# Kernel tuning notes

Measured on AMD Instinct MI355X. Metric: run time of the kernel, lower is better.

The kernel has to match this reference:

```python
import jax, jax.numpy as jnp
import numpy as np

EMBED = 1024
HEADS = 16
DH = EMBED // HEADS
B, S = 2, 2048


def setup_inputs() -> dict:
    key = jax.random.key(0)
    ks = jax.random.split(key, 12)
    inp = {
        "k": jax.random.normal(ks[0], (B, S, EMBED), jnp.float32),
        "q": jax.random.normal(ks[1], (B, S, EMBED), jnp.float32),
        "v": jax.random.normal(ks[2], (B, S, EMBED), jnp.float32),
        "mask": jax.random.randint(ks[3], (B, 1, S, S), 0, 2, jnp.int32),
        # per-head projections (shared across heads, as in the torch module)
        "Wk": jax.random.normal(ks[4], (DH, DH), jnp.float32) / np.sqrt(DH),
        "bk": jnp.zeros((DH,), jnp.float32),
        "Wq": jax.random.normal(ks[5], (DH, DH), jnp.float32) / np.sqrt(DH),
        "bq": jnp.zeros((DH,), jnp.float32),
        "Wv": jax.random.normal(ks[6], (DH, DH), jnp.float32) / np.sqrt(DH),
        "bv": jnp.zeros((DH,), jnp.float32),
        "Wo": jax.random.normal(ks[7], (EMBED, EMBED), jnp.float32) / np.sqrt(EMBED),
        "bo": jnp.zeros((EMBED,), jnp.float32),
    }
    return inp


def reference(k, q, v, mask, Wk, bk, Wq, bq, Wv, bv, Wo, bo):
    b, s, _ = k.shape
    sq = q.shape[1]
    # [B,S,H,dh]
    kh = k.reshape(b, s, HEADS, DH)
    qh = q.reshape(b, sq, HEADS, DH)
    vh = v.reshape(b, s, HEADS, DH)
    # per-head linear (weight shared across heads): x @ W.T + b
    kh = kh @ Wk.T + bk
    qh = qh @ Wq.T + bq
    vh = vh @ Wv.T + bv
    # scores [B,H,Sq,Sk]
    product = jnp.einsum("bqhd,bkhd->bhqk", qh, kh)
    # masked_fill BEFORE scaling, as in the original
    product = jnp.where(mask == 0, jnp.float32(-1e20), product)
    product = product / np.sqrt(DH)
    scores = jax.nn.softmax(product, axis=-1)
    ctx = jnp.einsum("bhqk,bkhd->bqhd", scores, vh).reshape(b, sq, EMBED)
    return ctx @ Wo.T + bo
```

## Files before the change

### kernel.cpp

```cpp
#include <hip/hip_runtime.h>
#include <hip/hip_bf16.h>
#include <math.h>

#define EMBED 1024
#define HEADS 16
#define DH    64
#define BATCH 2
#define SEQ   2048

typedef __attribute__((ext_vector_type(8))) short bf16x8;
typedef __attribute__((ext_vector_type(4))) short bf16x4;
typedef __attribute__((ext_vector_type(4))) float f32x4;
typedef unsigned long long u64;

#define QSCALE 0.1803368801111244f

static __device__ __forceinline__ unsigned short f2bf(float x) {
    unsigned u = __builtin_bit_cast(unsigned, x);
    return (unsigned short)((u + 0x7fffu + ((u >> 16) & 1u)) >> 16);
}
static __device__ __forceinline__ unsigned pk2bf(float a, float b) {
    union { __hip_bfloat162 h2; unsigned u; } c;
    c.h2 = __float22bfloat162_rn(make_float2(a, b));
    return c.u;
}
static __device__ __forceinline__ void gl_lds16(const void* g, void* l) {
    __builtin_amdgcn_global_load_lds(
        (const __attribute__((address_space(1))) void*)g,
        (__attribute__((address_space(3))) void*)l, 16, 0, 0);
}
static __device__ __forceinline__ bf16x8 cvt8(const float* p) {
    float4 a = ((const float4*)p)[0];
    float4 b = ((const float4*)p)[1];
    union { unsigned u[4]; bf16x8 v; } c;
    c.u[0] = pk2bf(a.x, a.y); c.u[1] = pk2bf(a.z, a.w);
    c.u[2] = pk2bf(b.x, b.y); c.u[3] = pk2bf(b.z, b.w);
    return c.v;
}

__global__ __launch_bounds__(256) void proj_mfma(
    const float* __restrict__ q, const float* __restrict__ k, const float* __restrict__ v,
    const float* __restrict__ Wq, const float* __restrict__ bq,
    const float* __restrict__ Wk, const float* __restrict__ bk,
    const float* __restrict__ Wv, const float* __restrict__ bv,
    unsigned short* __restrict__ qh, unsigned short* __restrict__ kh,
    unsigned short* __restrict__ vt,
    const int* __restrict__ mask, u64* __restrict__ bits,
    const float* __restrict__ Wo, unsigned short* __restrict__ Wob)
{
    const int blk   = blockIdx.x;
    const int which = blockIdx.y;
    const int t     = threadIdx.x;

    if (which == 3) {
        if (blk < 512) {
            const int idx = blk * 256 + t;
            const int4* src = (const int4*)(mask + (size_t)idx * 64);
            u64 wb = 0;
#pragma unroll
            for (int u = 0; u < 16; ++u) {
                int4 m = src[u];
                u64 nib = (m.x != 0 ? 1ull : 0) | (m.y != 0 ? 2ull : 0) |
                          (m.z != 0 ? 4ull : 0) | (m.w != 0 ? 8ull : 0);
                wb |= nib << (u * 4);
            }
            bits[idx] = wb;
        } else {
            const int i = ((blk - 512) * 256 + t) * 8;
            float4 a = ((const float4*)(Wo + i))[0];
            float4 b = ((const float4*)(Wo + i))[1];
            unsigned o32[4] = {pk2bf(a.x, a.y), pk2bf(a.z, a.w),
                               pk2bf(b.x, b.y), pk2bf(b.z, b.w)};
            *(uint4*)(Wob + i) = *(uint4*)o32;
        }
        return;
    }

    const float* x; const float* W; const float* bias;
    if (which == 0)      { x = q; W = Wq; bias = bq; }
    else if (which == 1) { x = k; W = Wk; bias = bk; }
    else                 { x = v; W = Wv; bias = bv; }

    __shared__ unsigned short Ws[64 * 72];

    const int w    = t >> 6;
    const int lane = t & 63;
    const int l15  = lane & 15;
    const int quad = lane >> 4;

    const int sr = t >> 2, sp = t & 3;
    {
        const float* wsrc = W + (size_t)sr * 64 + sp * 16;
        unsigned o32[8];
#pragma unroll
        for (int u4 = 0; u4 < 4; ++u4) {
            float4 a = ((const float4*)wsrc)[u4];
            o32[u4 * 2 + 0] = pk2bf(a.x, a.y);
            o32[u4 * 2 + 1] = pk2bf(a.z, a.w);
        }
        *(uint4*)&Ws[sr * 72 + sp * 16]     = *(uint4*)&o32[0];
        *(uint4*)&Ws[sr * 72 + sp * 16 + 8] = *(uint4*)&o32[4];
    }

    if (which == 2) {
        const int bh = blk >> 5;
        const int st = blk & 31;
        const int b  = bh >> 4, h = bh & 15;
        const int s  = st * 64 + w * 16 + l15;

        const float* xrow = x + ((size_t)(b * SEQ + s)) * EMBED + h * DH;
        const bf16x8 bx0 = cvt8(xrow + quad * 8);
        const bf16x8 bx1 = cvt8(xrow + 32 + quad * 8);

        __syncthreads();

#pragma unroll
        for (int nt = 0; nt < 4; ++nt) {
            bf16x8 aw0 = *(const bf16x8*)&Ws[(nt * 16 + l15) * 72 + quad * 8];
            bf16x8 aw1 = *(const bf16x8*)&Ws[(nt * 16 + l15) * 72 + 32 + quad * 8];
            f32x4 a = {0, 0, 0, 0};
            a = __builtin_amdgcn_mfma_f32_16x16x32_bf16(aw0, bx0, a, 0, 0, 0);
            a = __builtin_amdgcn_mfma_f32_16x16x32_bf16(aw1, bx1, a, 0, 0, 0);
#pragma unroll
            for (int r = 0; r < 4; ++r) {
                const int d = nt * 16 + quad * 4 + r;
                vt[((size_t)bh * DH + d) * SEQ + s] = f2bf(a[r] + bias[d]);
            }
        }
        return;
    }

    const float oscale = (which == 0) ? QSCALE : 1.0f;
    unsigned short* out = (which == 0) ? qh : kh;

    const float* xrow = x + ((size_t)blk * 64 + w * 16 + l15) * 64;
    const bf16x8 af0 = cvt8(xrow + quad * 8);
    const bf16x8 af1 = cvt8(xrow + 32 + quad * 8);

    __syncthreads();

    f32x4 acc[4];
#pragma unroll
    for (int nt = 0; nt < 4; ++nt) {
        bf16x8 bf0 = *(const bf16x8*)&Ws[(nt * 16 + l15) * 72 + quad * 8];
        bf16x8 bf1 = *(const bf16x8*)&Ws[(nt * 16 + l15) * 72 + 32 + quad * 8];
        f32x4 a = {0, 0, 0, 0};
        a = __builtin_amdgcn_mfma_f32_16x16x32_bf16(af0, bf0, a, 0, 0, 0);
        a = __builtin_amdgcn_mfma_f32_16x16x32_bf16(af1, bf1, a, 0, 0, 0);
        acc[nt] = a;
    }

    const int bsidx = blk * 4 + w;
    const int b = bsidx >> 11, s = bsidx & 2047;
#pragma unroll
    for (int nt = 0; nt < 4; ++nt) {
        const int d = nt * 16 + l15;
        const float bb = bias[d];
#pragma unroll
        for (int r = 0; r < 4; ++r) {
            const int h = quad * 4 + r;
            out[(((size_t)b * HEADS + h) * SEQ + s) * DH + d] =
                f2bf((acc[nt][r] + bb) * oscale);
        }
    }
}

__global__ __launch_bounds__(256, 4) void attn_kernel(
    const unsigned short* __restrict__ qh, const unsigned short* __restrict__ kh,
    const unsigned short* __restrict__ vt, const u64* __restrict__ mbits,
    unsigned short* __restrict__ ctx)
{
    const int bid = blockIdx.x;
    const int bh  = bid & 31;
    const int q0  = (bid >> 5) * 64;
    const int b   = bh >> 4;

    __shared__ unsigned char smem[32768];

    const int t    = threadIdx.x;
    const int w    = t >> 6;
    const int lane = t & 63;
    const int l15  = lane & 15;
    const int quad = lane >> 4;

    const int srow   = lane >> 3;
    const int schunk = (lane & 7) ^ srow;

    const unsigned short* qb = qh + ((size_t)bh * SEQ + q0 + w * 16 + l15) * DH + quad * 8;
    const bf16x8 qf0 = *(const bf16x8*)qb;
    const bf16x8 qf1 = *(const bf16x8*)(qb + 32);

    f32x4 O[4];
#pragma unroll
    for (int dt = 0; dt < 4; ++dt) O[dt] = f32x4{0, 0, 0, 0};
    f32x4 Osum = {0, 0, 0, 0};
    const bf16x4 ones = {(short)0x3F80, (short)0x3F80, (short)0x3F80, (short)0x3F80};

    const unsigned short* kbase = kh + (size_t)bh * SEQ * DH
                                  + (size_t)srow * DH + schunk * 8;
    const unsigned short* vbase = vt + (size_t)bh * DH * SEQ
                                  + (size_t)srow * SEQ + schunk * 8;
    const u64* mrow = mbits + ((size_t)b * SEQ + q0 + w * 16 + l15) * (SEQ / 64);

    if (w < 2) {
        unsigned char* Kd = smem;
#pragma unroll
        for (int j = 0; j < 4; ++j) {
            const int i = w * 4 + j;
            gl_lds16(kbase + (size_t)i * 8 * DH, Kd + i * 1024);
        }
    } else {
        unsigned char* Vd = smem + 8192;
#pragma unroll
        for (int j = 0; j < 4; ++j) {
            const int i = (w - 2) * 4 + j;
            gl_lds16(vbase + (size_t)i * 8 * SEQ, Vd + i * 1024);
        }
    }
    u64 pm = mrow[0];
    __syncthreads();

    for (int kt = 0; kt < 32; ++kt) {
        if (kt < 31) {
            const int bn = (kt + 1) & 1;
            if (w < 2) {
                unsigned char* Kd = smem + bn * 16384;
                const unsigned short* g0 = kbase + (size_t)(kt + 1) * 64 * DH;
#pragma unroll
                for (int j = 0; j < 4; ++j) {
                    const int i = w * 4 + j;
                    gl_lds16(g0 + (size_t)i * 8 * DH, Kd + i * 1024);
                }
            } else {
                unsigned char* Vd = smem + bn * 16384 + 8192;
                const unsigned short* g0 = vbase + (kt + 1) * 64;
#pragma unroll
                for (int j = 0; j < 4; ++j) {
                    const int i = (w - 2) * 4 + j;
                    gl_lds16(g0 + (size_t)i * 8 * SEQ, Vd + i * 1024);
                }
            }
        }
        const u64 mb = pm;
        if (kt < 31) pm = mrow[kt + 1];

        const unsigned short* KtH = (const unsigned short*)(smem + (kt & 1) * 16384);
        const unsigned short* VtH = KtH + 4096;

        const u64 mq = mb >> (quad * 4);
        bf16x4 p[4];
        const int rx = l15 & 7;
#pragma unroll
        for (int st = 0; st < 4; ++st) {
            const int r = st * 16 + l15;
            bf16x8 kf0 = *(const bf16x8*)&KtH[r * 64 + ((quad ^ rx)) * 8];
            bf16x8 kf1 = *(const bf16x8*)&KtH[r * 64 + ((quad ^ rx) ^ 4) * 8];
            f32x4 sa = {0, 0, 0, 0};
            sa = __builtin_amdgcn_mfma_f32_16x16x32_bf16(kf0, qf0, sa, 0, 0, 0);
            sa = __builtin_amdgcn_mfma_f32_16x16x32_bf16(kf1, qf1, sa, 0, 0, 0);
            const unsigned nib = (unsigned)(mq >> (st * 16)) & 0xFu;
            float p0 = (nib & 1u) ? exp2f(sa[0]) : 0.f;
            float p1 = (nib & 2u) ? exp2f(sa[1]) : 0.f;
            float p2 = (nib & 4u) ? exp2f(sa[2]) : 0.f;
            float p3 = (nib & 8u) ? exp2f(sa[3]) : 0.f;
            union { unsigned u2[2]; bf16x4 v; } pu;
            pu.u2[0] = pk2bf(p0, p1);
            pu.u2[1] = pk2bf(p2, p3);
            p[st] = pu.v;
            Osum = __builtin_amdgcn_mfma_f32_16x16x16bf16_1k(p[st], ones, Osum, 0, 0, 0);
        }

#pragma unroll
        for (int dt = 0; dt < 4; ++dt) {
            const int d = dt * 16 + l15;
            const int dx = l15 & 7;
#pragma unroll
            for (int st = 0; st < 4; ++st) {
                const int ch = (st * 2 + (quad >> 1)) ^ dx;
                bf16x4 vb = *(const bf16x4*)&VtH[d * 64 + ch * 8 + (quad & 1) * 4];
                O[dt] = __builtin_amdgcn_mfma_f32_16x16x16bf16_1k(p[st], vb, O[dt], 0, 0, 0);
            }
        }
        __syncthreads();
    }

    float inv[4];
#pragma unroll
    for (int r = 0; r < 4; ++r) inv[r] = 1.0f / Osum[r];
#pragma unroll
    for (int r = 0; r < 4; ++r) {
        const int row = q0 + w * 16 + quad * 4 + r;
        unsigned short* dst = ctx + ((size_t)bh * SEQ + row) * DH + l15;
#pragma unroll
        for (int dt = 0; dt < 4; ++dt)
            dst[dt * 16] = f2bf(O[dt][r] * inv[r]);
    }
}

__global__ __launch_bounds__(256, 4) void outproj_mfma(
    const unsigned short* __restrict__ ctx, const unsigned short* __restrict__ Wob,
    const float* __restrict__ bo, float* __restrict__ out)
{
    const int n0 = blockIdx.x * 64;
    const int m0 = blockIdx.y * 64;
    const int b  = m0 / SEQ;
    const int s0 = m0 % SEQ;

    __shared__ unsigned char smem[32768];

    const int t    = threadIdx.x;
    const int w    = t >> 6;
    const int lane = t & 63;
    const int l15  = lane & 15;
    const int quad = lane >> 4;
    const int srow   = lane >> 3;
    const int schunk = (lane & 7) ^ srow;

    const unsigned short* abase = ctx + ((size_t)b * HEADS * SEQ + s0 + srow) * DH + schunk * 8;
    const unsigned short* wbase = Wob + (size_t)(n0 + srow) * EMBED + schunk * 8;

    f32x4 acc[4] = {f32x4{0,0,0,0}, f32x4{0,0,0,0}, f32x4{0,0,0,0}, f32x4{0,0,0,0}};

    {
        unsigned char* Ab = smem;
        unsigned char* Wb = smem + 8192;
#pragma unroll
        for (int j = 0; j < 4; ++j) {
            const int idx = w * 4 + j;
            if (idx < 8)
                gl_lds16(abase + (size_t)idx * 8 * DH, Ab + idx * 1024);
            else
                gl_lds16(wbase + (size_t)(idx - 8) * 8 * EMBED, Wb + (idx - 8) * 1024);
        }
    }
    __syncthreads();

    for (int kt = 0; kt < 16; ++kt) {
        if (kt < 15) {
            const int ktn = kt + 1;
            unsigned char* Ab = smem + (ktn & 1) * 16384;
            unsigned char* Wb = Ab + 8192;
#pragma unroll
            for (int j = 0; j < 4; ++j) {
                const int idx = w * 4 + j;
                if (idx < 8)
                    gl_lds16(abase + (size_t)ktn * SEQ * DH + (size_t)idx * 8 * DH,
                             Ab + idx * 1024);
                else
                    gl_lds16(wbase + (size_t)(idx - 8) * 8 * EMBED + ktn * 64,
                             Wb + (idx - 8) * 1024);
            }
        }

        const unsigned short* At = (const unsigned short*)(smem + (kt & 1) * 16384);
        const unsigned short* Wt = At + 4096;
        const int rx = l15 & 7;
        const int c0 = ((quad ^ rx)) * 8;

        bf16x8 bf0 = *(const bf16x8*)&Wt[(w * 16 + l15) * 64 + c0];
        bf16x8 bf1 = *(const bf16x8*)&Wt[(w * 16 + l15) * 64 + (c0 ^ 32)];
#pragma unroll
        for (int mt = 0; mt < 4; ++mt) {
            bf16x8 af0 = *(const bf16x8*)&At[(mt * 16 + l15) * 64 + c0];
            bf16x8 af1 = *(const bf16x8*)&At[(mt * 16 + l15) * 64 + (c0 ^ 32)];
            acc[mt] = __builtin_amdgcn_mfma_f32_16x16x32_bf16(af0, bf0, acc[mt], 0, 0, 0);
            acc[mt] = __builtin_amdgcn_mfma_f32_16x16x32_bf16(af1, bf1, acc[mt], 0, 0, 0);
        }
        __syncthreads();
    }

    const float bv = bo[n0 + w * 16 + l15];
#pragma unroll
    for (int mt = 0; mt < 4; ++mt) {
#pragma unroll
        for (int r = 0; r < 4; ++r) {
            out[(size_t)(m0 + mt * 16 + quad * 4 + r) * EMBED + n0 + w * 16 + l15] =
                acc[mt][r] + bv;
        }
    }
}

extern "C" void kernel_launch(void* const* d_in, const int* in_sizes, int n_in,
                              void* d_out, int out_size, void* d_ws, size_t ws_size,
                              hipStream_t stream) {
    const float* k    = (const float*)d_in[0];
    const float* q    = (const float*)d_in[1];
    const float* v    = (const float*)d_in[2];
    const int*   mask = (const int*)  d_in[3];
    const float* Wk   = (const float*)d_in[4];
    const float* bk   = (const float*)d_in[5];
    const float* Wq   = (const float*)d_in[6];
    const float* bq   = (const float*)d_in[7];
    const float* Wv   = (const float*)d_in[8];
    const float* bv   = (const float*)d_in[9];
    const float* Wo   = (const float*)d_in[10];
    const float* bo   = (const float*)d_in[11];
    float* out = (float*)d_out;

    const size_t TEN = (size_t)BATCH * HEADS * SEQ * DH;
    unsigned short* qh_bf = (unsigned short*)d_ws;
    unsigned short* kh_bf = qh_bf + TEN;
    unsigned short* vt_bf = kh_bf + TEN;
    unsigned short* ctxb  = vt_bf + TEN;
    unsigned short* Wob   = ctxb + TEN;
    u64*            mbits = (u64*)(Wob + EMBED * EMBED);

    proj_mfma<<<dim3(1024, 4), 256, 0, stream>>>(
        q, k, v, Wq, bq, Wk, bk, Wv, bv,
        qh_bf, kh_bf, vt_bf, mask, mbits, Wo, Wob);
    attn_kernel<<<dim3((SEQ / 64) * BATCH * HEADS), 256, 0, stream>>>(
        qh_bf, kh_bf, vt_bf, mbits, ctxb);
    outproj_mfma<<<dim3(EMBED / 64, BATCH * SEQ / 64), 256, 0, stream>>>(
        ctxb, Wob, bo, out);
}
```

Measured before the change: 240.0 us.

## Pre-swizzle K into MFMA fragment layout and read it directly from global

The projection kernel now writes K in a packed layout laid out per 16-row group and 8-column chunk, so that each lane of the attention kernel can load its MFMA operand fragments straight from global memory (through L2/L1) instead of staging K tiles in LDS. Only V remains double-buffered in LDS, which halves the shared-memory footprint and the number of async copies per iteration. The compute section is also wrapped in s_setprio to raise wave priority. The cost is that K loads now come from cache with no software prefetch, so global load latency may be exposed in the QK step.

```diff
diff --git a/kernel.cpp b/kernel.cpp
--- a/kernel.cpp
+++ b/kernel.cpp
@@ -43,7 +43,7 @@
     const float* __restrict__ Wq, const float* __restrict__ bq,
     const float* __restrict__ Wk, const float* __restrict__ bk,
     const float* __restrict__ Wv, const float* __restrict__ bv,
-    unsigned short* __restrict__ qh, unsigned short* __restrict__ kh,
+    unsigned short* __restrict__ qh, unsigned short* __restrict__ Kp,
     unsigned short* __restrict__ vt,
     const int* __restrict__ mask, u64* __restrict__ bits,
     const float* __restrict__ Wo, unsigned short* __restrict__ Wob)
@@ -131,7 +131,6 @@
     }
 
     const float oscale = (which == 0) ? QSCALE : 1.0f;
-    unsigned short* out = (which == 0) ? qh : kh;
 
     const float* xrow = x + ((size_t)blk * 64 + w * 16 + l15) * 64;
     const bf16x8 af0 = cvt8(xrow + quad * 8);
@@ -152,21 +151,38 @@
 
     const int bsidx = blk * 4 + w;
     const int b = bsidx >> 11, s = bsidx & 2047;
-#pragma unroll
-    for (int nt = 0; nt < 4; ++nt) {
-        const int d = nt * 16 + l15;
-        const float bb = bias[d];
-#pragma unroll
-        for (int r = 0; r < 4; ++r) {
-            const int h = quad * 4 + r;
-            out[(((size_t)b * HEADS + h) * SEQ + s) * DH + d] =
-                f2bf((acc[nt][r] + bb) * oscale);
+
+    if (which == 0) {
+#pragma unroll
+        for (int nt = 0; nt < 4; ++nt) {
+            const int d = nt * 16 + l15;
+            const float bb = bias[d];
+#pragma unroll
+            for (int r = 0; r < 4; ++r) {
+                const int h = quad * 4 + r;
+                qh[(((size_t)b * HEADS + h) * SEQ + s) * DH + d] =
+                    f2bf((acc[nt][r] + bb) * oscale);
+            }
+        }
+    } else {
+        const int sg = s >> 4, sr16 = s & 15;
+#pragma unroll
+        for (int nt = 0; nt < 4; ++nt) {
+            const int d  = nt * 16 + l15;
+            const int dc = d >> 3, d7 = d & 7;
+            const float bb = bias[d];
+#pragma unroll
+            for (int r = 0; r < 4; ++r) {
+                const int h = quad * 4 + r;
+                Kp[(((size_t)(b * HEADS + h) * 128 + sg) * 8 + dc) * 128
+                   + sr16 * 8 + d7] = f2bf(acc[nt][r] + bb);
+            }
         }
     }
 }
 
 __global__ __launch_bounds__(256, 4) void attn_kernel(
-    const unsigned short* __restrict__ qh, const unsigned short* __restrict__ kh,
+    const unsigned short* __restrict__ qh, const unsigned short* __restrict__ Kp,
     const unsigned short* __restrict__ vt, const u64* __restrict__ mbits,
     unsigned short* __restrict__ ctx)
 {
@@ -175,7 +191,7 @@
     const int q0  = (bid >> 5) * 64;
     const int b   = bh >> 4;
 
-    __shared__ unsigned char smem[32768];
+    __shared__ unsigned char smem[16384];
 
     const int t    = threadIdx.x;
     const int w    = t >> 6;
@@ -196,24 +212,17 @@
     f32x4 Osum = {0, 0, 0, 0};
     const bf16x4 ones = {(short)0x3F80, (short)0x3F80, (short)0x3F80, (short)0x3F80};
 
-    const unsigned short* kbase = kh + (size_t)bh * SEQ * DH
-                                  + (size_t)srow * DH + schunk * 8;
+    const unsigned short* kp = Kp + (size_t)bh * 128 * 1024 + lane * 8;
+
     const unsigned short* vbase = vt + (size_t)bh * DH * SEQ
                                   + (size_t)srow * SEQ + schunk * 8;
     const u64* mrow = mbits + ((size_t)b * SEQ + q0 + w * 16 + l15) * (SEQ / 64);
 
-    if (w < 2) {
-        unsigned char* Kd = smem;
-#pragma unroll
-        for (int j = 0; j < 4; ++j) {
-            const int i = w * 4 + j;
-            gl_lds16(kbase + (size_t)i * 8 * DH, Kd + i * 1024);
-        }
-    } else {
-        unsigned char* Vd = smem + 8192;
-#pragma unroll
-        for (int j = 0; j < 4; ++j) {
-            const int i = (w - 2) * 4 + j;
+    {
+        unsigned char* Vd = smem;
+#pragma unroll
+        for (int j = 0; j < 2; ++j) {
+            const int i = w * 2 + j;
             gl_lds16(vbase + (size_t)i * 8 * SEQ, Vd + i * 1024);
         }
     }
@@ -222,39 +231,28 @@
 
     for (int kt = 0; kt < 32; ++kt) {
         if (kt < 31) {
-            const int bn = (kt + 1) & 1;
-            if (w < 2) {
-                unsigned char* Kd = smem + bn * 16384;
-                const unsigned short* g0 = kbase + (size_t)(kt + 1) * 64 * DH;
-#pragma unroll
-                for (int j = 0; j < 4; ++j) {
-                    const int i = w * 4 + j;
-                    gl_lds16(g0 + (size_t)i * 8 * DH, Kd + i * 1024);
-                }
-            } else {
-                unsigned char* Vd = smem + bn * 16384 + 8192;
-                const unsigned short* g0 = vbase + (kt + 1) * 64;
-#pragma unroll
-                for (int j = 0; j < 4; ++j) {
-                    const int i = (w - 2) * 4 + j;
-                    gl_lds16(g0 + (size_t)i * 8 * SEQ, Vd + i * 1024);
-                }
+            unsigned char* Vd = smem + ((kt + 1) & 1) * 8192;
+            const unsigned short* g0 = vbase + (kt + 1) * 64;
+#pragma unroll
+            for (int j = 0; j < 2; ++j) {
+                const int i = w * 2 + j;
+                gl_lds16(g0 + (size_t)i * 8 * SEQ, Vd + i * 1024);
             }
         }
         const u64 mb = pm;
         if (kt < 31) pm = mrow[kt + 1];
 
-        const unsigned short* KtH = (const unsigned short*)(smem + (kt & 1) * 16384);
-        const unsigned short* VtH = KtH + 4096;
+        const unsigned short* VtH = (const unsigned short*)(smem + (kt & 1) * 8192);
+        const unsigned short* kpt = kp + (size_t)kt * 4 * 1024;
+
+        __builtin_amdgcn_s_setprio(1);
 
         const u64 mq = mb >> (quad * 4);
         bf16x4 p[4];
-        const int rx = l15 & 7;
 #pragma unroll
         for (int st = 0; st < 4; ++st) {
-            const int r = st * 16 + l15;
-            bf16x8 kf0 = *(const bf16x8*)&KtH[r * 64 + ((quad ^ rx)) * 8];
-            bf16x8 kf1 = *(const bf16x8*)&KtH[r * 64 + ((quad ^ rx) ^ 4) * 8];
+            bf16x8 kf0 = *(const bf16x8*)&kpt[st * 1024];
+            bf16x8 kf1 = *(const bf16x8*)&kpt[st * 1024 + 512];
             f32x4 sa = {0, 0, 0, 0};
             sa = __builtin_amdgcn_mfma_f32_16x16x32_bf16(kf0, qf0, sa, 0, 0, 0);
             sa = __builtin_amdgcn_mfma_f32_16x16x32_bf16(kf1, qf1, sa, 0, 0, 0);
@@ -281,6 +279,7 @@
                 O[dt] = __builtin_amdgcn_mfma_f32_16x16x16bf16_1k(p[st], vb, O[dt], 0, 0, 0);
             }
         }
+        __builtin_amdgcn_s_setprio(0);
         __syncthreads();
     }
 
@@ -399,17 +398,17 @@
 
     const size_t TEN = (size_t)BATCH * HEADS * SEQ * DH;
     unsigned short* qh_bf = (unsigned short*)d_ws;
-    unsigned short* kh_bf = qh_bf + TEN;
-    unsigned short* vt_bf = kh_bf + TEN;
+    unsigned short* kp_bf = qh_bf + TEN;
+    unsigned short* vt_bf = kp_bf + TEN;
     unsigned short* ctxb  = vt_bf + TEN;
     unsigned short* Wob   = ctxb + TEN;
     u64*            mbits = (u64*)(Wob + EMBED * EMBED);
 
     proj_mfma<<<dim3(1024, 4), 256, 0, stream>>>(
         q, k, v, Wq, bq, Wk, bk, Wv, bv,
-        qh_bf, kh_bf, vt_bf, mask, mbits, Wo, Wob);
+        qh_bf, kp_bf, vt_bf, mask, mbits, Wo, Wob);
     attn_kernel<<<dim3((SEQ / 64) * BATCH * HEADS), 256, 0, stream>>>(
-        qh_bf, kh_bf, vt_bf, mbits, ctxb);
+        qh_bf, kp_bf, vt_bf, mbits, ctxb);
     outproj_mfma<<<dim3(EMBED / 64, BATCH * SEQ / 64), 256, 0, stream>>>(
         ctxb, Wob, bo, out);
 }
```

Measured after the change: 243.6 us. About the same (+1.5%).

## Pre-pack V into MFMA fragment order and load it straight to registers

Applied to the files above, without the earlier changes.

The V projection now writes its output in a tiled layout that matches the MFMA B-fragment order for each 64-key tile. The attention kernel reads V fragments directly from global memory into registers instead of staging them through LDS, which halves the shared memory footprint and removes the V LDS writes and reads. The cost is that all four waves read the same V tile redundantly from global or L2 each iteration, and these loads sit on the critical path instead of being prefetched a tile ahead.

```diff
diff --git a/kernel.cpp b/kernel.cpp
--- a/kernel.cpp
+++ b/kernel.cpp
@@ -44,7 +44,7 @@
     const float* __restrict__ Wk, const float* __restrict__ bk,
     const float* __restrict__ Wv, const float* __restrict__ bv,
     unsigned short* __restrict__ qh, unsigned short* __restrict__ kh,
-    unsigned short* __restrict__ vt,
+    unsigned short* __restrict__ Vp,
     const int* __restrict__ mask, u64* __restrict__ bits,
     const float* __restrict__ Wo, unsigned short* __restrict__ Wob)
 {
@@ -104,9 +104,9 @@
 
     if (which == 2) {
         const int bh = blk >> 5;
-        const int st = blk & 31;
+        const int kt = blk & 31;
         const int b  = bh >> 4, h = bh & 15;
-        const int s  = st * 64 + w * 16 + l15;
+        const int s  = kt * 64 + w * 16 + l15;
 
         const float* xrow = x + ((size_t)(b * SEQ + s)) * EMBED + h * DH;
         const bf16x8 bx0 = cvt8(xrow + quad * 8);
@@ -114,6 +114,8 @@
 
         __syncthreads();
 
+        unsigned short* vtile = Vp + ((size_t)bh * 32 + kt) * 4096;
+        const int qr = l15 >> 2, j = l15 & 3;
 #pragma unroll
         for (int nt = 0; nt < 4; ++nt) {
             bf16x8 aw0 = *(const bf16x8*)&Ws[(nt * 16 + l15) * 72 + quad * 8];
@@ -124,7 +126,8 @@
 #pragma unroll
             for (int r = 0; r < 4; ++r) {
                 const int d = nt * 16 + quad * 4 + r;
-                vt[((size_t)bh * DH + d) * SEQ + s] = f2bf(a[r] + bias[d]);
+                vtile[((w * 4 + nt) * 64 + qr * 16 + quad * 4 + r) * 4 + j] =
+                    f2bf(a[r] + bias[d]);
             }
         }
         return;
@@ -167,7 +170,7 @@
 
 __global__ __launch_bounds__(256, 4) void attn_kernel(
     const unsigned short* __restrict__ qh, const unsigned short* __restrict__ kh,
-    const unsigned short* __restrict__ vt, const u64* __restrict__ mbits,
+    const unsigned short* __restrict__ Vp, const u64* __restrict__ mbits,
     unsigned short* __restrict__ ctx)
 {
     const int bid = blockIdx.x;
@@ -175,7 +178,7 @@
     const int q0  = (bid >> 5) * 64;
     const int b   = bh >> 4;
 
-    __shared__ unsigned char smem[32768];
+    __shared__ unsigned char smem[16384];
 
     const int t    = threadIdx.x;
     const int w    = t >> 6;
@@ -198,23 +201,15 @@
 
     const unsigned short* kbase = kh + (size_t)bh * SEQ * DH
                                   + (size_t)srow * DH + schunk * 8;
-    const unsigned short* vbase = vt + (size_t)bh * DH * SEQ
-                                  + (size_t)srow * SEQ + schunk * 8;
+    const unsigned short* vfrag = Vp + (size_t)bh * 32 * 4096 + lane * 4;
     const u64* mrow = mbits + ((size_t)b * SEQ + q0 + w * 16 + l15) * (SEQ / 64);
 
-    if (w < 2) {
+    {
         unsigned char* Kd = smem;
 #pragma unroll
-        for (int j = 0; j < 4; ++j) {
-            const int i = w * 4 + j;
+        for (int j = 0; j < 2; ++j) {
+            const int i = w * 2 + j;
             gl_lds16(kbase + (size_t)i * 8 * DH, Kd + i * 1024);
-        }
-    } else {
-        unsigned char* Vd = smem + 8192;
-#pragma unroll
-        for (int j = 0; j < 4; ++j) {
-            const int i = (w - 2) * 4 + j;
-            gl_lds16(vbase + (size_t)i * 8 * SEQ, Vd + i * 1024);
         }
     }
     u64 pm = mrow[0];
@@ -222,30 +217,26 @@
 
     for (int kt = 0; kt < 32; ++kt) {
         if (kt < 31) {
-            const int bn = (kt + 1) & 1;
-            if (w < 2) {
-                unsigned char* Kd = smem + bn * 16384;
-                const unsigned short* g0 = kbase + (size_t)(kt + 1) * 64 * DH;
-#pragma unroll
-                for (int j = 0; j < 4; ++j) {
-                    const int i = w * 4 + j;
-                    gl_lds16(g0 + (size_t)i * 8 * DH, Kd + i * 1024);
-                }
-            } else {
-                unsigned char* Vd = smem + bn * 16384 + 8192;
-                const unsigned short* g0 = vbase + (kt + 1) * 64;
-#pragma unroll
-                for (int j = 0; j < 4; ++j) {
-                    const int i = (w - 2) * 4 + j;
-                    gl_lds16(g0 + (size_t)i * 8 * SEQ, Vd + i * 1024);
-                }
+            unsigned char* Kd = smem + ((kt + 1) & 1) * 8192;
+            const unsigned short* g0 = kbase + (size_t)(kt + 1) * 64 * DH;
+#pragma unroll
+            for (int j = 0; j < 2; ++j) {
+                const int i = w * 2 + j;
+                gl_lds16(g0 + (size_t)i * 8 * DH, Kd + i * 1024);
             }
         }
+        const unsigned short* vt0 = vfrag + (size_t)kt * 4096;
+        bf16x4 vb[4][4];
+#pragma unroll
+        for (int st = 0; st < 4; ++st)
+#pragma unroll
+            for (int dt = 0; dt < 4; ++dt)
+                vb[dt][st] = *(const bf16x4*)&vt0[(st * 4 + dt) * 256];
+
         const u64 mb = pm;
         if (kt < 31) pm = mrow[kt + 1];
 
-        const unsigned short* KtH = (const unsigned short*)(smem + (kt & 1) * 16384);
-        const unsigned short* VtH = KtH + 4096;
+        const unsigned short* KtH = (const unsigned short*)(smem + (kt & 1) * 8192);
 
         const u64 mq = mb >> (quad * 4);
         bf16x4 p[4];
@@ -271,16 +262,11 @@
         }
 
 #pragma unroll
-        for (int dt = 0; dt < 4; ++dt) {
-            const int d = dt * 16 + l15;
-            const int dx = l15 & 7;
-#pragma unroll
-            for (int st = 0; st < 4; ++st) {
-                const int ch = (st * 2 + (quad >> 1)) ^ dx;
-                bf16x4 vb = *(const bf16x4*)&VtH[d * 64 + ch * 8 + (quad & 1) * 4];
-                O[dt] = __builtin_amdgcn_mfma_f32_16x16x16bf16_1k(p[st], vb, O[dt], 0, 0, 0);
-            }
-        }
+        for (int dt = 0; dt < 4; ++dt)
+#pragma unroll
+            for (int st = 0; st < 4; ++st)
+                O[dt] = __builtin_amdgcn_mfma_f32_16x16x16bf16_1k(p[st], vb[dt][st], O[dt], 0, 0, 0);
+
         __syncthreads();
     }
 
@@ -400,16 +386,16 @@
     const size_t TEN = (size_t)BATCH * HEADS * SEQ * DH;
     unsigned short* qh_bf = (unsigned short*)d_ws;
     unsigned short* kh_bf = qh_bf + TEN;
-    unsigned short* vt_bf = kh_bf + TEN;
-    unsigned short* ctxb  = vt_bf + TEN;
+    unsigned short* vp_bf = kh_bf + TEN;
+    unsigned short* ctxb  = vp_bf + TEN;
     unsigned short* Wob   = ctxb + TEN;
     u64*            mbits = (u64*)(Wob + EMBED * EMBED);
 
     proj_mfma<<<dim3(1024, 4), 256, 0, stream>>>(
         q, k, v, Wq, bq, Wk, bk, Wv, bv,
-        qh_bf, kh_bf, vt_bf, mask, mbits, Wo, Wob);
+        qh_bf, kh_bf, vp_bf, mask, mbits, Wo, Wob);
     attn_kernel<<<dim3((SEQ / 64) * BATCH * HEADS), 256, 0, stream>>>(
-        qh_bf, kh_bf, vt_bf, mbits, ctxb);
+        qh_bf, kh_bf, vp_bf, mbits, ctxb);
     outproj_mfma<<<dim3(EMBED / 64, BATCH * SEQ / 64), 256, 0, stream>>>(
         ctxb, Wob, bo, out);
 }
```

Result: slower. 250.3 us (+4.3%).
